# Performance work log

Measured on AMD Instinct MI355X. Metric: run time of the kernel, lower is better.

Reference implementation:

```python
import jax, jax.numpy as jnp
import numpy as np

N_NODES = 100000
N_EDGES = 1000000
IN_FEATS = 64
HID = 128
NUM_CLASSES = 10


def setup_inputs() -> dict:
    key = jax.random.key(0)
    ks = jax.random.split(key, 8)
    x = jax.random.normal(ks[0], (N_NODES, IN_FEATS), dtype=jnp.float32)
    edge_index = jax.random.randint(ks[1], (2, N_EDGES), 0, N_NODES, dtype=jnp.int64)
    # Glorot-style init scale for weights
    def w(k, fan_in, fan_out):
        s = (2.0 / (fan_in + fan_out)) ** 0.5
        return jax.random.normal(k, (fan_in, fan_out), dtype=jnp.float32) * s
    return {
        "x": x,
        "edge_index": edge_index,
        "W1": w(ks[2], IN_FEATS, HID),
        "b1": jnp.zeros((HID,), dtype=jnp.float32),
        "W2": w(ks[3], HID, HID),
        "b2": jnp.zeros((HID,), dtype=jnp.float32),
        "Wl": w(ks[4], HID, NUM_CLASSES),
        "bl": jnp.zeros((NUM_CLASSES,), dtype=jnp.float32),
    }


def _gcn_conv(x, src, dst, norm, W, b, num_nodes):
    # PyG GCNConv: h = x W, then out_i = sum_{j->i} norm_ij * h_j + b
    h = x @ W  # [N, out]
    msgs = h[src] * norm[:, None]  # gather + scale  [E+N, out]
    out = jax.ops.segment_sum(msgs, dst, num_segments=num_nodes)
    return out + b


def reference(x, edge_index, W1, b1, W2, b2, Wl, bl):
    N = x.shape[0]
    loops = jnp.arange(N, dtype=edge_index.dtype)
    src = jnp.concatenate([edge_index[0], loops])  # source nodes (messages from)
    dst = jnp.concatenate([edge_index[1], loops])  # target nodes (aggregate at)
    # symmetric normalization: deg over targets (includes self-loops)
    deg = jax.ops.segment_sum(jnp.ones(dst.shape, dtype=x.dtype), dst, num_segments=N)
    dinv = jnp.where(deg > 0, jax.lax.rsqrt(deg), 0.0)
    norm = dinv[src] * dinv[dst]  # [E+N]

    h = jax.nn.relu(_gcn_conv(x, src, dst, norm, W1, b1, N))
    h = jax.nn.relu(_gcn_conv(h, src, dst, norm, W2, b2, N))
    return jax.nn.log_softmax(h @ Wl + bl, axis=1)
```

## Files before the change

kernel.cpp:

```cpp
#include <hip/hip_runtime.h>
#include <hip/hip_fp16.h>
#include <math.h>

#define NUM_CLASSES 10

#define BSH 7
#define BSZ 128
#define BCAP 1792
#define NBMAX 1024
#define P1BATCH 4096
#define PREPB 97

typedef _Float16 half8  __attribute__((ext_vector_type(8)));
typedef _Float16 half4t __attribute__((ext_vector_type(4)));
typedef float    floatx4 __attribute__((ext_vector_type(4)));

__global__ __launch_bounds__(256) void prep_p1_kernel(const float* __restrict__ W1,
                                                      const float* __restrict__ W2,
                                                      const float* __restrict__ Wlc,
                                                      _Float16* __restrict__ W1t,
                                                      _Float16* __restrict__ W2t,
                                                      _Float16* __restrict__ Wct,
                                                      const int* __restrict__ src,
                                                      const int* __restrict__ dst,
                                                      int* __restrict__ bucket_fill,
                                                      unsigned* __restrict__ pairs, int E) {
    __shared__ int hist[NBMAX], base[NBMAX], cur[NBMAX];
    const int tid = threadIdx.x;
    const int b = blockIdx.x;

    if (b < PREPB) {
        if (b < 32) {
            int i = b * 256 + tid;
            int k = i >> 7, c = i & 127;
            W1t[c * 72 + k] = (_Float16)W1[i];
        } else if (b < 96) {
            int i = (b - 32) * 256 + tid;
            int k = i >> 7, c = i & 127;
            W2t[c * 136 + k] = (_Float16)W2[i];
        } else {
            for (int i = tid; i < 16 * 136; i += 256) {
                int c = i / 136, k = i - c * 136;
                float v = (c < NUM_CLASSES && k < 128) ? Wlc[k * NUM_CLASSES + c] : 0.0f;
                Wct[i] = (_Float16)v;
            }
        }
        return;
    }

    for (int i = tid; i < NBMAX; i += 256) { hist[i] = 0; cur[i] = 0; }
    __syncthreads();
    const int bb = (b - PREPB) * P1BATCH;
    unsigned pk[16];
    int bk[16];
    int cnt = 0;
#pragma unroll
    for (int i = 0; i < 16; ++i) {
        int idx = bb + i * 256 + tid;
        if (idx < E) {
            int s = src[idx], d = dst[idx];
            bk[i] = d >> BSH;
            pk[i] = ((unsigned)s << BSH) | (unsigned)(d & (BSZ - 1));
            atomicAdd(&hist[bk[i]], 1);
            cnt = i + 1;
        }
    }
    __syncthreads();
    for (int i = tid; i < NBMAX; i += 256)
        if (hist[i] > 0) base[i] = atomicAdd(&bucket_fill[i], hist[i]);
    __syncthreads();
#pragma unroll
    for (int i = 0; i < 16; ++i) {
        if (i < cnt) {
            int bi = bk[i];
            int r = atomicAdd(&cur[bi], 1) + base[bi];
            if (r < BCAP) pairs[(size_t)bi * BCAP + r] = pk[i];
        }
    }
}

__global__ __launch_bounds__(256) void csr_p2_kernel(const int* __restrict__ bucket_fill,
                                                     const unsigned* __restrict__ pairs,
                                                     const float* __restrict__ x,
                                                     int* __restrict__ rowstart,
                                                     float* __restrict__ dinv,
                                                     int* __restrict__ csr_src,
                                                     __half2* __restrict__ xs_h,
                                                     int N, int nbuck) {
    __shared__ int cnt[BSZ], excl[BSZ], cur[BSZ];
    __shared__ int s1[256];
    const int tid = threadIdx.x;
    const int b = blockIdx.x;
    const int node0 = b << BSH;
    const int nodes_b = min(BSZ, N - node0);

    if (tid < BSZ) { cnt[tid] = 0; cur[tid] = 0; }
    int part = 0;
    for (int j = tid; j < b; j += 256) part += bucket_fill[j];
    s1[tid] = part;
    __syncthreads();
    for (int off = 128; off > 0; off >>= 1) {
        if (tid < off) s1[tid] += s1[tid + off];
        __syncthreads();
    }
    const int bbase = s1[0];
    const int ne = bucket_fill[b];
    __syncthreads();

    const unsigned* bp = pairs + (size_t)b * BCAP;
    for (int i = tid; i < ne; i += 256)
        atomicAdd(&cnt[bp[i] & (BSZ - 1)], 1);
    __syncthreads();
    int c = (tid < BSZ) ? cnt[tid] : 0;
    if (tid < BSZ) s1[tid] = c;
    __syncthreads();
    for (int off = 1; off < BSZ; off <<= 1) {
        int t = (tid < BSZ && tid >= off) ? s1[tid - off] : 0;
        __syncthreads();
        if (tid < BSZ) s1[tid] += t;
        __syncthreads();
    }
    if (tid < BSZ) excl[tid] = s1[tid] - c;
    __syncthreads();

    if (tid < nodes_b) {
        rowstart[node0 + tid] = bbase + excl[tid];
        dinv[node0 + tid] = rsqrtf((float)cnt[tid] + 1.0f);
    }
    if (b == nbuck - 1 && tid == 0) rowstart[N] = bbase + ne;

    for (int i = tid; i < nodes_b * 32; i += 256) {
        int ln = i >> 5;
        float d = rsqrtf((float)cnt[ln] + 1.0f);
        float2 v = ((const float2*)x)[(size_t)node0 * 32 + i];
        xs_h[(size_t)node0 * 32 + i] = __floats2half2_rn(v.x * d, v.y * d);
    }
    for (int i = tid; i < ne; i += 256) {
        unsigned p = bp[i];
        int d = (int)(p & (BSZ - 1));
        int r = atomicAdd(&cur[d], 1);
        csr_src[bbase + excl[d] + r] = (int)(p >> BSH);
    }
}

__global__ __launch_bounds__(256) void gather64_kernel(const __half2* __restrict__ xs,
                                                       const float* __restrict__ dinv,
                                                       const int* __restrict__ rowstart,
                                                       const int* __restrict__ csr_src,
                                                       __half2* __restrict__ out, int N) {
    int node = (blockIdx.x * 256 + threadIdx.x) >> 6;
    int lane = threadIdx.x & 63;
    if (node >= N) return;
    int f2 = lane & 31;

    int beg = rowstart[node];
    int end = rowstart[node + 1];
    int deg = end - beg;

    float2 self = __half22float2(xs[(size_t)node * 32 + f2]);
    float2 acc;

    if (deg <= 16) {
        int myidx = (lane < deg) ? csr_src[beg + lane] : node;
        float comp = (float)(deg - 15);
        acc.x = self.x * comp;
        acc.y = self.y * comp;
        float2 v[16];
#pragma unroll
        for (int u = 0; u < 16; ++u) {
            int s = __shfl(myidx, u);
            v[u] = __half22float2(xs[(size_t)s * 32 + f2]);
        }
#pragma unroll
        for (int u = 0; u < 16; ++u) { acc.x += v[u].x; acc.y += v[u].y; }
    } else {
        int lim = deg < 64 ? deg : 64;
        int myidx = (lane < lim) ? csr_src[beg + lane] : node;
        int itersUp = (lim + 7) & ~7;
        float comp = (float)(1 - (itersUp - lim));
        acc.x = self.x * comp;
        acc.y = self.y * comp;
        for (int j = 0; j < itersUp; j += 8) {
            int s[8];
#pragma unroll
            for (int u = 0; u < 8; ++u) s[u] = __shfl(myidx, j + u);
            float2 v[8];
#pragma unroll
            for (int u = 0; u < 8; ++u) v[u] = __half22float2(xs[(size_t)s[u] * 32 + f2]);
#pragma unroll
            for (int u = 0; u < 8; ++u) { acc.x += v[u].x; acc.y += v[u].y; }
        }
        for (int j = beg + 64; j < end; ++j) {
            float2 v = __half22float2(xs[(size_t)csr_src[j] * 32 + f2]);
            acc.x += v.x;
            acc.y += v.y;
        }
    }
    if (lane < 32) {
        float d = dinv[node];
        out[(size_t)node * 32 + f2] = __floats2half2_rn(d * acc.x, d * acc.y);
    }
}

__global__ __launch_bounds__(256) void gather128_kernel(const __half2* __restrict__ hs,
                                                        const float* __restrict__ dinv,
                                                        const int* __restrict__ rowstart,
                                                        const int* __restrict__ csr_src,
                                                        __half2* __restrict__ out, int N) {
    int node = (blockIdx.x * 256 + threadIdx.x) >> 6;
    int lane = threadIdx.x & 63;
    if (node >= N) return;

    int beg = rowstart[node];
    int end = rowstart[node + 1];
    int deg = end - beg;

    float2 self = __half22float2(hs[(size_t)node * 64 + lane]);
    int lim = deg < 64 ? deg : 64;
    int myidx = (lane < lim) ? csr_src[beg + lane] : node;
    int itersUp = (lim + 7) & ~7;
    float comp = (float)(1 - (itersUp - lim));
    float2 acc;
    acc.x = self.x * comp;
    acc.y = self.y * comp;

    for (int j = 0; j < itersUp; j += 8) {
        int s[8];
#pragma unroll
        for (int u = 0; u < 8; ++u) s[u] = __shfl(myidx, j + u);
        float2 v[8];
#pragma unroll
        for (int u = 0; u < 8; ++u) v[u] = __half22float2(hs[(size_t)s[u] * 64 + lane]);
#pragma unroll
        for (int u = 0; u < 8; ++u) { acc.x += v[u].x; acc.y += v[u].y; }
    }
    for (int j = beg + 64; j < end; ++j) {
        float2 v = __half22float2(hs[(size_t)csr_src[j] * 64 + lane]);
        acc.x += v.x;
        acc.y += v.y;
    }
    float d = dinv[node];
    out[(size_t)node * 64 + lane] = __floats2half2_rn(d * acc.x, d * acc.y);
}

template <int K, bool SCALE_OUT>
__global__ __launch_bounds__(256) void gemm_mfma_kernel(const _Float16* __restrict__ In,
                                                        const _Float16* __restrict__ Wt,
                                                        const float* __restrict__ bias,
                                                        const float* __restrict__ dinv,
                                                        _Float16* __restrict__ Out, int N) {
    constexpr int KP = K + 8;
    constexpr int NC = K / 32;
    __shared__ _Float16 Wl[128 * KP];
    __shared__ float bias_s[128];
    const int tid = threadIdx.x;

    for (int i = tid; i < (128 * KP) / 8; i += 256)
        ((floatx4*)Wl)[i] = ((const floatx4*)Wt)[i];
    if (tid < 128) bias_s[tid] = bias[tid];
    __syncthreads();

    const int lane = tid & 63;
    const int wave = tid >> 6;
    const int q = lane >> 4;
    const int l15 = lane & 15;

#pragma unroll
    for (int iter = 0; iter < 2; ++iter) {
        int myrow = blockIdx.x * 128 + iter * 64 + wave * 16 + l15;
        int r = myrow < N ? myrow : N - 1;
        half8 xf[NC];
#pragma unroll
        for (int c = 0; c < NC; ++c)
            xf[c] = *(const half8*)(In + (size_t)r * K + c * 32 + q * 8);
        floatx4 acc[8];
#pragma unroll
        for (int t = 0; t < 8; ++t) acc[t] = (floatx4){0.f, 0.f, 0.f, 0.f};
#pragma unroll
        for (int c = 0; c < NC; ++c) {
#pragma unroll
            for (int t = 0; t < 8; ++t) {
                half8 wf = *(const half8*)(Wl + (t * 16 + l15) * KP + c * 32 + q * 8);
                acc[t] = __builtin_amdgcn_mfma_f32_16x16x32_f16(wf, xf[c], acc[t], 0, 0, 0);
            }
        }
        if (myrow < N) {
            float sc = SCALE_OUT ? dinv[myrow] : 1.0f;
#pragma unroll
            for (int t = 0; t < 8; ++t) {
                int c0 = t * 16 + q * 4;
                floatx4 bv = *(const floatx4*)&bias_s[c0];
                half4t hh;
#pragma unroll
                for (int j = 0; j < 4; ++j)
                    hh[j] = (_Float16)(sc * fmaxf(acc[t][j] + bv[j], 0.0f));
                *(half4t*)(Out + (size_t)myrow * 128 + c0) = hh;
            }
        }
    }
}

__global__ __launch_bounds__(256) void gemm_final_kernel(const _Float16* __restrict__ In,
                                                         const _Float16* __restrict__ Wt,
                                                         const float* __restrict__ bias,
                                                         const _Float16* __restrict__ Wct,
                                                         const float* __restrict__ bl,
                                                         float* __restrict__ out, int N) {
    constexpr int K = 128, KP = 136, NC = 4;
    __shared__ _Float16 Wl[128 * KP];
    __shared__ _Float16 Wc[16 * KP];
    __shared__ float bias_s[128];
    __shared__ float bl_s[16];
    __shared__ _Float16 act_s[4][16 * KP];
    const int tid = threadIdx.x;

    for (int i = tid; i < (128 * KP) / 8; i += 256)
        ((floatx4*)Wl)[i] = ((const floatx4*)Wt)[i];
    for (int i = tid; i < (16 * KP) / 8; i += 256)
        ((floatx4*)Wc)[i] = ((const floatx4*)Wct)[i];
    if (tid < 128) bias_s[tid] = bias[tid];
    if (tid < 16) bl_s[tid] = (tid < NUM_CLASSES) ? bl[tid] : -1e30f;
    __syncthreads();

    const int lane = tid & 63;
    const int wave = tid >> 6;
    const int q = lane >> 4;
    const int l15 = lane & 15;
    _Float16* As = act_s[wave];

    half8 wcf[NC];
#pragma unroll
    for (int c = 0; c < NC; ++c)
        wcf[c] = *(const half8*)(Wc + l15 * KP + c * 32 + q * 8);
    float myclsb[4];
#pragma unroll
    for (int reg = 0; reg < 4; ++reg) myclsb[reg] = bl_s[q * 4 + reg];

#pragma unroll
    for (int iter = 0; iter < 2; ++iter) {
        int myrow = blockIdx.x * 128 + iter * 64 + wave * 16 + l15;
        int r = myrow < N ? myrow : N - 1;
        half8 xf[NC];
#pragma unroll
        for (int c = 0; c < NC; ++c)
            xf[c] = *(const half8*)(In + (size_t)r * K + c * 32 + q * 8);
        floatx4 acc[8];
#pragma unroll
        for (int t = 0; t < 8; ++t) acc[t] = (floatx4){0.f, 0.f, 0.f, 0.f};
#pragma unroll
        for (int c = 0; c < NC; ++c) {
#pragma unroll
            for (int t = 0; t < 8; ++t) {
                half8 wf = *(const half8*)(Wl + (t * 16 + l15) * KP + c * 32 + q * 8);
                acc[t] = __builtin_amdgcn_mfma_f32_16x16x32_f16(wf, xf[c], acc[t], 0, 0, 0);
            }
        }
#pragma unroll
        for (int t = 0; t < 8; ++t) {
            int c0 = t * 16 + q * 4;
            floatx4 bv = *(const floatx4*)&bias_s[c0];
            half4t hh;
#pragma unroll
            for (int j = 0; j < 4; ++j)
                hh[j] = (_Float16)fmaxf(acc[t][j] + bv[j], 0.0f);
            *(half4t*)&As[l15 * KP + c0] = hh;
        }
        floatx4 lg = (floatx4){0.f, 0.f, 0.f, 0.f};
#pragma unroll
        for (int c = 0; c < NC; ++c) {
            half8 af = *(const half8*)(As + l15 * KP + c * 32 + q * 8);
            lg = __builtin_amdgcn_mfma_f32_16x16x32_f16(wcf[c], af, lg, 0, 0, 0);
        }
        if (myrow < N) {
            float v[4];
#pragma unroll
            for (int reg = 0; reg < 4; ++reg) v[reg] = lg[reg] + myclsb[reg];
            float mx = fmaxf(fmaxf(v[0], v[1]), fmaxf(v[2], v[3]));
            mx = fmaxf(mx, __shfl_xor(mx, 16));
            mx = fmaxf(mx, __shfl_xor(mx, 32));
            float sm = expf(v[0] - mx) + expf(v[1] - mx) + expf(v[2] - mx) + expf(v[3] - mx);
            sm += __shfl_xor(sm, 16);
            sm += __shfl_xor(sm, 32);
            float lse = mx + logf(sm);
#pragma unroll
            for (int reg = 0; reg < 4; ++reg) {
                int cls = q * 4 + reg;
                if (cls < NUM_CLASSES)
                    out[(size_t)myrow * NUM_CLASSES + cls] = v[reg] - lse;
            }
        }
    }
}

extern "C" void kernel_launch(void* const* d_in, const int* in_sizes, int n_in,
                              void* d_out, int out_size, void* d_ws, size_t ws_size,
                              hipStream_t stream) {
    const float* x  = (const float*)d_in[0];
    const int*   ei = (const int*)d_in[1];
    const float* W1 = (const float*)d_in[2];
    const float* b1 = (const float*)d_in[3];
    const float* W2 = (const float*)d_in[4];
    const float* b2 = (const float*)d_in[5];
    const float* Wlc = (const float*)d_in[6];
    const float* bl = (const float*)d_in[7];
    float* out = (float*)d_out;

    const int N = in_sizes[0] / 64;
    const int E = in_sizes[1] / 2;
    const int* src = ei;
    const int* dst = ei + E;
    const int nbuck = (N + BSZ - 1) >> BSH;

    char* ws = (char*)d_ws;
    int*      bucket_fill = (int*)(ws + 0);
    int*      rowstart    = (int*)(ws + 4096);
    float*    dinv        = (float*)(ws + 524288);
    _Float16* W1t         = (_Float16*)(ws + 1048576);
    _Float16* W2t         = (_Float16*)(ws + 1069056);
    _Float16* Wct         = (_Float16*)(ws + 1103872);
    unsigned* pairs       = (unsigned*)(ws + 2097152);
    int*      csr_src     = (int*)(ws + 12582912);
    __half2*  xs_h        = (__half2*)(ws + 16777216);
    __half2*  g1h         = (__half2*)(ws + 33554432);
    __half2*  g2h         = (__half2*)(ws + 46923776);
    __half2*  a1_h        = (__half2*)(ws + 73400320);

    const int P1B = (E + P1BATCH - 1) / P1BATCH;
    const int GB  = (N + 127) / 128;
    const int WVB = (N + 3) / 4;

    hipMemsetAsync(bucket_fill, 0, nbuck * sizeof(int), stream);
    prep_p1_kernel<<<PREPB + P1B, 256, 0, stream>>>(W1, W2, Wlc, W1t, W2t, Wct,
                                                    src, dst, bucket_fill, pairs, E);
    csr_p2_kernel<<<nbuck, 256, 0, stream>>>(bucket_fill, pairs, x, rowstart, dinv,
                                             csr_src, xs_h, N, nbuck);

    gather64_kernel<<<WVB, 256, 0, stream>>>(xs_h, dinv, rowstart, csr_src, g1h, N);
    gemm_mfma_kernel<64, true><<<GB, 256, 0, stream>>>((const _Float16*)g1h, W1t, b1, dinv,
                                                       (_Float16*)a1_h, N);

    gather128_kernel<<<WVB, 256, 0, stream>>>(a1_h, dinv, rowstart, csr_src, g2h, N);
    gemm_final_kernel<<<GB, 256, 0, stream>>>((const _Float16*)g2h, W2t, b2, Wct, bl, out, N);
}
```

Before: 224.9 us.

## Fuse layer-1 gather with its MFMA GEMM through shared memory

Merges the 64-wide neighbor gather and the first-layer GEMM into one kernel. Each 512-thread block has its 8 waves gather 16 nodes each into an LDS tile, then runs the MFMA GEMM on that tile. This removes the g1h round trip through global memory and one kernel launch. In exchange, each wave now handles 16 nodes sequentially instead of one wave per node, which cuts the parallelism available to hide gather latency, and each block uses more LDS.

```diff
diff --git a/kernel.cpp b/kernel.cpp
--- a/kernel.cpp
+++ b/kernel.cpp
@@ -143,62 +143,115 @@
     }
 }
 
-__global__ __launch_bounds__(256) void gather64_kernel(const __half2* __restrict__ xs,
-                                                       const float* __restrict__ dinv,
-                                                       const int* __restrict__ rowstart,
-                                                       const int* __restrict__ csr_src,
-                                                       __half2* __restrict__ out, int N) {
-    int node = (blockIdx.x * 256 + threadIdx.x) >> 6;
-    int lane = threadIdx.x & 63;
-    if (node >= N) return;
-    int f2 = lane & 31;
-
-    int beg = rowstart[node];
-    int end = rowstart[node + 1];
-    int deg = end - beg;
-
-    float2 self = __half22float2(xs[(size_t)node * 32 + f2]);
-    float2 acc;
-
-    if (deg <= 16) {
-        int myidx = (lane < deg) ? csr_src[beg + lane] : node;
-        float comp = (float)(deg - 15);
-        acc.x = self.x * comp;
-        acc.y = self.y * comp;
-        float2 v[16];
-#pragma unroll
-        for (int u = 0; u < 16; ++u) {
-            int s = __shfl(myidx, u);
-            v[u] = __half22float2(xs[(size_t)s * 32 + f2]);
-        }
-#pragma unroll
-        for (int u = 0; u < 16; ++u) { acc.x += v[u].x; acc.y += v[u].y; }
-    } else {
-        int lim = deg < 64 ? deg : 64;
-        int myidx = (lane < lim) ? csr_src[beg + lane] : node;
-        int itersUp = (lim + 7) & ~7;
-        float comp = (float)(1 - (itersUp - lim));
-        acc.x = self.x * comp;
-        acc.y = self.y * comp;
-        for (int j = 0; j < itersUp; j += 8) {
-            int s[8];
-#pragma unroll
-            for (int u = 0; u < 8; ++u) s[u] = __shfl(myidx, j + u);
-            float2 v[8];
-#pragma unroll
-            for (int u = 0; u < 8; ++u) v[u] = __half22float2(xs[(size_t)s[u] * 32 + f2]);
-#pragma unroll
-            for (int u = 0; u < 8; ++u) { acc.x += v[u].x; acc.y += v[u].y; }
-        }
-        for (int j = beg + 64; j < end; ++j) {
-            float2 v = __half22float2(xs[(size_t)csr_src[j] * 32 + f2]);
-            acc.x += v.x;
-            acc.y += v.y;
-        }
-    }
-    if (lane < 32) {
-        float d = dinv[node];
-        out[(size_t)node * 32 + f2] = __floats2half2_rn(d * acc.x, d * acc.y);
+__global__ __launch_bounds__(512) void gather_gemm64_kernel(const __half2* __restrict__ xs,
+                                                            const float* __restrict__ dinv,
+                                                            const int* __restrict__ rowstart,
+                                                            const int* __restrict__ csr_src,
+                                                            const _Float16* __restrict__ Wt,
+                                                            const float* __restrict__ bias,
+                                                            _Float16* __restrict__ Out, int N) {
+    constexpr int KP = 72;
+    __shared__ _Float16 Wl[128 * KP];
+    __shared__ _Float16 As[128 * KP];
+    __shared__ float bias_s[128];
+    const int tid = threadIdx.x;
+
+    for (int i = tid; i < (128 * KP) / 8; i += 512)
+        ((floatx4*)Wl)[i] = ((const floatx4*)Wt)[i];
+    if (tid < 128) bias_s[tid] = bias[tid];
+
+    const int lane = tid & 63;
+    const int wave = tid >> 6;
+    const int f2 = lane & 31;
+
+    const int nbase = blockIdx.x * 128 + wave * 16;
+    for (int nn = 0; nn < 16; ++nn) {
+        int node = nbase + nn;
+        if (node >= N) break;
+
+        int beg = rowstart[node];
+        int end = rowstart[node + 1];
+        int deg = end - beg;
+
+        float2 self = __half22float2(xs[(size_t)node * 32 + f2]);
+        float2 acc;
+
+        if (deg <= 16) {
+            int myidx = (lane < deg) ? csr_src[beg + lane] : node;
+            float comp = (float)(deg - 15);
+            acc.x = self.x * comp;
+            acc.y = self.y * comp;
+            float2 v[16];
+#pragma unroll
+            for (int u = 0; u < 16; ++u) {
+                int s = __shfl(myidx, u);
+                v[u] = __half22float2(xs[(size_t)s * 32 + f2]);
+            }
+#pragma unroll
+            for (int u = 0; u < 16; ++u) { acc.x += v[u].x; acc.y += v[u].y; }
+        } else {
+            int lim = deg < 64 ? deg : 64;
+            int myidx = (lane < lim) ? csr_src[beg + lane] : node;
+            int itersUp = (lim + 7) & ~7;
+            float comp = (float)(1 - (itersUp - lim));
+            acc.x = self.x * comp;
+            acc.y = self.y * comp;
+            for (int j = 0; j < itersUp; j += 8) {
+                int s[8];
+#pragma unroll
+                for (int u = 0; u < 8; ++u) s[u] = __shfl(myidx, j + u);
+                float2 v[8];
+#pragma unroll
+                for (int u = 0; u < 8; ++u) v[u] = __half22float2(xs[(size_t)s[u] * 32 + f2]);
+#pragma unroll
+                for (int u = 0; u < 8; ++u) { acc.x += v[u].x; acc.y += v[u].y; }
+            }
+            for (int j = beg + 64; j < end; ++j) {
+                float2 v = __half22float2(xs[(size_t)csr_src[j] * 32 + f2]);
+                acc.x += v.x;
+                acc.y += v.y;
+            }
+        }
+        if (lane < 32) {
+            float d = dinv[node];
+            *(__half2*)(As + (wave * 16 + nn) * KP + f2 * 2) =
+                __floats2half2_rn(d * acc.x, d * acc.y);
+        }
+    }
+    __syncthreads();
+
+    const int q = lane >> 4;
+    const int l15 = lane & 15;
+    const int lrow = wave * 16 + l15;
+    const int myrow = blockIdx.x * 128 + lrow;
+
+    half8 xf[2];
+#pragma unroll
+    for (int c = 0; c < 2; ++c)
+        xf[c] = *(const half8*)(As + lrow * KP + c * 32 + q * 8);
+    floatx4 acc8[8];
+#pragma unroll
+    for (int t = 0; t < 8; ++t) acc8[t] = (floatx4){0.f, 0.f, 0.f, 0.f};
+#pragma unroll
+    for (int c = 0; c < 2; ++c) {
+#pragma unroll
+        for (int t = 0; t < 8; ++t) {
+            half8 wf = *(const half8*)(Wl + (t * 16 + l15) * KP + c * 32 + q * 8);
+            acc8[t] = __builtin_amdgcn_mfma_f32_16x16x32_f16(wf, xf[c], acc8[t], 0, 0, 0);
+        }
+    }
+    if (myrow < N) {
+        float sc = dinv[myrow];
+#pragma unroll
+        for (int t = 0; t < 8; ++t) {
+            int c0 = t * 16 + q * 4;
+            floatx4 bv = *(const floatx4*)&bias_s[c0];
+            half4t hh;
+#pragma unroll
+            for (int j = 0; j < 4; ++j)
+                hh[j] = (_Float16)(sc * fmaxf(acc8[t][j] + bv[j], 0.0f));
+            *(half4t*)(Out + (size_t)myrow * 128 + c0) = hh;
+        }
     }
 }
 
@@ -241,63 +294,6 @@
     }
     float d = dinv[node];
     out[(size_t)node * 64 + lane] = __floats2half2_rn(d * acc.x, d * acc.y);
-}
-
-template <int K, bool SCALE_OUT>
-__global__ __launch_bounds__(256) void gemm_mfma_kernel(const _Float16* __restrict__ In,
-                                                        const _Float16* __restrict__ Wt,
-                                                        const float* __restrict__ bias,
-                                                        const float* __restrict__ dinv,
-                                                        _Float16* __restrict__ Out, int N) {
-    constexpr int KP = K + 8;
-    constexpr int NC = K / 32;
-    __shared__ _Float16 Wl[128 * KP];
-    __shared__ float bias_s[128];
-    const int tid = threadIdx.x;
-
-    for (int i = tid; i < (128 * KP) / 8; i += 256)
-        ((floatx4*)Wl)[i] = ((const floatx4*)Wt)[i];
-    if (tid < 128) bias_s[tid] = bias[tid];
-    __syncthreads();
-
-    const int lane = tid & 63;
-    const int wave = tid >> 6;
-    const int q = lane >> 4;
-    const int l15 = lane & 15;
-
-#pragma unroll
-    for (int iter = 0; iter < 2; ++iter) {
-        int myrow = blockIdx.x * 128 + iter * 64 + wave * 16 + l15;
-        int r = myrow < N ? myrow : N - 1;
-        half8 xf[NC];
-#pragma unroll
-        for (int c = 0; c < NC; ++c)
-            xf[c] = *(const half8*)(In + (size_t)r * K + c * 32 + q * 8);
-        floatx4 acc[8];
-#pragma unroll
-        for (int t = 0; t < 8; ++t) acc[t] = (floatx4){0.f, 0.f, 0.f, 0.f};
-#pragma unroll
-        for (int c = 0; c < NC; ++c) {
-#pragma unroll
-            for (int t = 0; t < 8; ++t) {
-                half8 wf = *(const half8*)(Wl + (t * 16 + l15) * KP + c * 32 + q * 8);
-                acc[t] = __builtin_amdgcn_mfma_f32_16x16x32_f16(wf, xf[c], acc[t], 0, 0, 0);
-            }
-        }
-        if (myrow < N) {
-            float sc = SCALE_OUT ? dinv[myrow] : 1.0f;
-#pragma unroll
-            for (int t = 0; t < 8; ++t) {
-                int c0 = t * 16 + q * 4;
-                floatx4 bv = *(const floatx4*)&bias_s[c0];
-                half4t hh;
-#pragma unroll
-                for (int j = 0; j < 4; ++j)
-                    hh[j] = (_Float16)(sc * fmaxf(acc[t][j] + bv[j], 0.0f));
-                *(half4t*)(Out + (size_t)myrow * 128 + c0) = hh;
-            }
-        }
-    }
 }
 
 __global__ __launch_bounds__(256) void gemm_final_kernel(const _Float16* __restrict__ In,
@@ -421,7 +417,6 @@
     unsigned* pairs       = (unsigned*)(ws + 2097152);
     int*      csr_src     = (int*)(ws + 12582912);
     __half2*  xs_h        = (__half2*)(ws + 16777216);
-    __half2*  g1h         = (__half2*)(ws + 33554432);
     __half2*  g2h         = (__half2*)(ws + 46923776);
     __half2*  a1_h        = (__half2*)(ws + 73400320);
 
@@ -435,9 +430,8 @@
     csr_p2_kernel<<<nbuck, 256, 0, stream>>>(bucket_fill, pairs, x, rowstart, dinv,
                                              csr_src, xs_h, N, nbuck);
 
-    gather64_kernel<<<WVB, 256, 0, stream>>>(xs_h, dinv, rowstart, csr_src, g1h, N);
-    gemm_mfma_kernel<64, true><<<GB, 256, 0, stream>>>((const _Float16*)g1h, W1t, b1, dinv,
-                                                       (_Float16*)a1_h, N);
+    gather_gemm64_kernel<<<GB, 512, 0, stream>>>(xs_h, dinv, rowstart, csr_src,
+                                                 W1t, b1, (_Float16*)a1_h, N);
 
     gather128_kernel<<<WVB, 256, 0, stream>>>(a1_h, dinv, rowstart, csr_src, g2h, N);
     gemm_final_kernel<<<GB, 256, 0, stream>>>((const _Float16*)g2h, W2t, b2, Wct, bl, out, N);
```

Result: slower. 243.2 us (+8.1%).

## Fuse layer-2 neighbor gather with final GEMM and log-softmax kernel

Applied to the files above, without the earlier changes.

Merges the second-layer gather kernel with the final GEMM+classifier kernel. Each block gathers 16 nodes into shared memory, then runs the W2 MFMA product (split across 4 waves) and the classifier plus log-softmax on one wave. This removes the round trip of the 128-wide gathered activations through global memory and one kernel launch. In exchange, weights are read from global/L2 per block instead of staged in LDS, the block count grows to N/16, and gather parallelism per block drops while barriers serialize gather and compute phases.

```diff
diff --git a/kernel.cpp b/kernel.cpp
--- a/kernel.cpp
+++ b/kernel.cpp
@@ -202,47 +202,6 @@
     }
 }
 
-__global__ __launch_bounds__(256) void gather128_kernel(const __half2* __restrict__ hs,
-                                                        const float* __restrict__ dinv,
-                                                        const int* __restrict__ rowstart,
-                                                        const int* __restrict__ csr_src,
-                                                        __half2* __restrict__ out, int N) {
-    int node = (blockIdx.x * 256 + threadIdx.x) >> 6;
-    int lane = threadIdx.x & 63;
-    if (node >= N) return;
-
-    int beg = rowstart[node];
-    int end = rowstart[node + 1];
-    int deg = end - beg;
-
-    float2 self = __half22float2(hs[(size_t)node * 64 + lane]);
-    int lim = deg < 64 ? deg : 64;
-    int myidx = (lane < lim) ? csr_src[beg + lane] : node;
-    int itersUp = (lim + 7) & ~7;
-    float comp = (float)(1 - (itersUp - lim));
-    float2 acc;
-    acc.x = self.x * comp;
-    acc.y = self.y * comp;
-
-    for (int j = 0; j < itersUp; j += 8) {
-        int s[8];
-#pragma unroll
-        for (int u = 0; u < 8; ++u) s[u] = __shfl(myidx, j + u);
-        float2 v[8];
-#pragma unroll
-        for (int u = 0; u < 8; ++u) v[u] = __half22float2(hs[(size_t)s[u] * 64 + lane]);
-#pragma unroll
-        for (int u = 0; u < 8; ++u) { acc.x += v[u].x; acc.y += v[u].y; }
-    }
-    for (int j = beg + 64; j < end; ++j) {
-        float2 v = __half22float2(hs[(size_t)csr_src[j] * 64 + lane]);
-        acc.x += v.x;
-        acc.y += v.y;
-    }
-    float d = dinv[node];
-    out[(size_t)node * 64 + lane] = __floats2half2_rn(d * acc.x, d * acc.y);
-}
-
 template <int K, bool SCALE_OUT>
 __global__ __launch_bounds__(256) void gemm_mfma_kernel(const _Float16* __restrict__ In,
                                                         const _Float16* __restrict__ Wt,
@@ -300,81 +259,104 @@
     }
 }
 
-__global__ __launch_bounds__(256) void gemm_final_kernel(const _Float16* __restrict__ In,
-                                                         const _Float16* __restrict__ Wt,
-                                                         const float* __restrict__ bias,
-                                                         const _Float16* __restrict__ Wct,
-                                                         const float* __restrict__ bl,
-                                                         float* __restrict__ out, int N) {
-    constexpr int K = 128, KP = 136, NC = 4;
-    __shared__ _Float16 Wl[128 * KP];
-    __shared__ _Float16 Wc[16 * KP];
-    __shared__ float bias_s[128];
-    __shared__ float bl_s[16];
-    __shared__ _Float16 act_s[4][16 * KP];
+__global__ __launch_bounds__(256) void gather_gemm_final_kernel(
+        const __half2* __restrict__ hs,
+        const float* __restrict__ dinv,
+        const int* __restrict__ rowstart,
+        const int* __restrict__ csr_src,
+        const _Float16* __restrict__ Wt,
+        const float* __restrict__ bias,
+        const _Float16* __restrict__ Wct,
+        const float* __restrict__ bl,
+        float* __restrict__ out, int N) {
+    constexpr int KP = 136;
+    __shared__ _Float16 As[16 * KP];
+    __shared__ _Float16 H2[16 * KP];
     const int tid = threadIdx.x;
-
-    for (int i = tid; i < (128 * KP) / 8; i += 256)
-        ((floatx4*)Wl)[i] = ((const floatx4*)Wt)[i];
-    for (int i = tid; i < (16 * KP) / 8; i += 256)
-        ((floatx4*)Wc)[i] = ((const floatx4*)Wct)[i];
-    if (tid < 128) bias_s[tid] = bias[tid];
-    if (tid < 16) bl_s[tid] = (tid < NUM_CLASSES) ? bl[tid] : -1e30f;
-    __syncthreads();
-
     const int lane = tid & 63;
     const int wave = tid >> 6;
+
+    for (int nn = 0; nn < 4; ++nn) {
+        const int r = wave * 4 + nn;
+        const int node = blockIdx.x * 16 + r;
+        if (node < N) {
+            int beg = rowstart[node];
+            int end = rowstart[node + 1];
+            int deg = end - beg;
+
+            float2 self = __half22float2(hs[(size_t)node * 64 + lane]);
+            int lim = deg < 64 ? deg : 64;
+            int myidx = (lane < lim) ? csr_src[beg + lane] : node;
+            int itersUp = (lim + 7) & ~7;
+            float comp = (float)(1 - (itersUp - lim));
+            float2 acc;
+            acc.x = self.x * comp;
+            acc.y = self.y * comp;
+
+            for (int j = 0; j < itersUp; j += 8) {
+                int s[8];
+#pragma unroll
+                for (int u = 0; u < 8; ++u) s[u] = __shfl(myidx, j + u);
+                float2 v[8];
+#pragma unroll
+                for (int u = 0; u < 8; ++u) v[u] = __half22float2(hs[(size_t)s[u] * 64 + lane]);
+#pragma unroll
+                for (int u = 0; u < 8; ++u) { acc.x += v[u].x; acc.y += v[u].y; }
+            }
+            for (int j = beg + 64; j < end; ++j) {
+                float2 v = __half22float2(hs[(size_t)csr_src[j] * 64 + lane]);
+                acc.x += v.x;
+                acc.y += v.y;
+            }
+            float d = dinv[node];
+            ((__half2*)As)[r * 68 + lane] = __floats2half2_rn(d * acc.x, d * acc.y);
+        }
+    }
+    __syncthreads();
+
     const int q = lane >> 4;
     const int l15 = lane & 15;
-    _Float16* As = act_s[wave];
-
-    half8 wcf[NC];
-#pragma unroll
-    for (int c = 0; c < NC; ++c)
-        wcf[c] = *(const half8*)(Wc + l15 * KP + c * 32 + q * 8);
-    float myclsb[4];
-#pragma unroll
-    for (int reg = 0; reg < 4; ++reg) myclsb[reg] = bl_s[q * 4 + reg];
-
-#pragma unroll
-    for (int iter = 0; iter < 2; ++iter) {
-        int myrow = blockIdx.x * 128 + iter * 64 + wave * 16 + l15;
-        int r = myrow < N ? myrow : N - 1;
-        half8 xf[NC];
-#pragma unroll
-        for (int c = 0; c < NC; ++c)
-            xf[c] = *(const half8*)(In + (size_t)r * K + c * 32 + q * 8);
-        floatx4 acc[8];
-#pragma unroll
-        for (int t = 0; t < 8; ++t) acc[t] = (floatx4){0.f, 0.f, 0.f, 0.f};
-#pragma unroll
-        for (int c = 0; c < NC; ++c) {
-#pragma unroll
-            for (int t = 0; t < 8; ++t) {
-                half8 wf = *(const half8*)(Wl + (t * 16 + l15) * KP + c * 32 + q * 8);
-                acc[t] = __builtin_amdgcn_mfma_f32_16x16x32_f16(wf, xf[c], acc[t], 0, 0, 0);
-            }
-        }
-#pragma unroll
-        for (int t = 0; t < 8; ++t) {
-            int c0 = t * 16 + q * 4;
-            floatx4 bv = *(const floatx4*)&bias_s[c0];
-            half4t hh;
-#pragma unroll
-            for (int j = 0; j < 4; ++j)
-                hh[j] = (_Float16)fmaxf(acc[t][j] + bv[j], 0.0f);
-            *(half4t*)&As[l15 * KP + c0] = hh;
-        }
+
+    half8 xf[4];
+#pragma unroll
+    for (int c = 0; c < 4; ++c)
+        xf[c] = *(const half8*)(As + l15 * KP + c * 32 + q * 8);
+
+#pragma unroll
+    for (int tt = 0; tt < 2; ++tt) {
+        const int t = wave * 2 + tt;
+        floatx4 acc = (floatx4){0.f, 0.f, 0.f, 0.f};
+#pragma unroll
+        for (int c = 0; c < 4; ++c) {
+            half8 wf = *(const half8*)(Wt + (t * 16 + l15) * KP + c * 32 + q * 8);
+            acc = __builtin_amdgcn_mfma_f32_16x16x32_f16(wf, xf[c], acc, 0, 0, 0);
+        }
+        const int c0 = t * 16 + q * 4;
+        floatx4 bv = *(const floatx4*)(bias + c0);
+        half4t hh;
+#pragma unroll
+        for (int j = 0; j < 4; ++j)
+            hh[j] = (_Float16)fmaxf(acc[j] + bv[j], 0.0f);
+        *(half4t*)&H2[l15 * KP + c0] = hh;
+    }
+    __syncthreads();
+
+    if (wave == 0) {
         floatx4 lg = (floatx4){0.f, 0.f, 0.f, 0.f};
 #pragma unroll
-        for (int c = 0; c < NC; ++c) {
-            half8 af = *(const half8*)(As + l15 * KP + c * 32 + q * 8);
-            lg = __builtin_amdgcn_mfma_f32_16x16x32_f16(wcf[c], af, lg, 0, 0, 0);
-        }
+        for (int c = 0; c < 4; ++c) {
+            half8 wcf = *(const half8*)(Wct + l15 * KP + c * 32 + q * 8);
+            half8 af = *(const half8*)(H2 + l15 * KP + c * 32 + q * 8);
+            lg = __builtin_amdgcn_mfma_f32_16x16x32_f16(wcf, af, lg, 0, 0, 0);
+        }
+        const int myrow = blockIdx.x * 16 + l15;
         if (myrow < N) {
             float v[4];
 #pragma unroll
-            for (int reg = 0; reg < 4; ++reg) v[reg] = lg[reg] + myclsb[reg];
+            for (int reg = 0; reg < 4; ++reg) {
+                int cls = q * 4 + reg;
+                v[reg] = lg[reg] + ((cls < NUM_CLASSES) ? bl[cls] : -1e30f);
+            }
             float mx = fmaxf(fmaxf(v[0], v[1]), fmaxf(v[2], v[3]));
             mx = fmaxf(mx, __shfl_xor(mx, 16));
             mx = fmaxf(mx, __shfl_xor(mx, 32));
@@ -422,12 +404,12 @@
     int*      csr_src     = (int*)(ws + 12582912);
     __half2*  xs_h        = (__half2*)(ws + 16777216);
     __half2*  g1h         = (__half2*)(ws + 33554432);
-    __half2*  g2h         = (__half2*)(ws + 46923776);
     __half2*  a1_h        = (__half2*)(ws + 73400320);
 
     const int P1B = (E + P1BATCH - 1) / P1BATCH;
     const int GB  = (N + 127) / 128;
     const int WVB = (N + 3) / 4;
+    const int FGB = (N + 15) / 16;
 
     hipMemsetAsync(bucket_fill, 0, nbuck * sizeof(int), stream);
     prep_p1_kernel<<<PREPB + P1B, 256, 0, stream>>>(W1, W2, Wlc, W1t, W2t, Wct,
@@ -439,6 +421,6 @@
     gemm_mfma_kernel<64, true><<<GB, 256, 0, stream>>>((const _Float16*)g1h, W1t, b1, dinv,
                                                        (_Float16*)a1_h, N);
 
-    gather128_kernel<<<WVB, 256, 0, stream>>>(a1_h, dinv, rowstart, csr_src, g2h, N);
-    gemm_final_kernel<<<GB, 256, 0, stream>>>((const _Float16*)g2h, W2t, b2, Wct, bl, out, N);
-}
+    gather_gemm_final_kernel<<<FGB, 256, 0, stream>>>(a1_h, dinv, rowstart, csr_src,
+                                                      W2t, b2, Wct, bl, out, N);
+}
```

Measured after the change: 218.2 us. 3.0% less time.
